# Kernel tuning notes

Measured on AMD Instinct MI355X. Metric: run time of the kernel, lower is better.

## Reference

```python
import jax, jax.numpy as jnp
import numpy as np

HID = 1024
DEPTH = 2

def _rhn_layer(x, Win, bin_, Wh, bh, Wt, bt):
    # x: [B, T, in]; returns outputs [B, T, H]
    B = x.shape[0]
    h0 = jnp.zeros((B, HID), dtype=x.dtype)
    xt = jnp.swapaxes(x, 0, 1)  # [T, B, in]

    def step(h_prev, x_t):
        h = x_t @ Win + bin_
        for i in range(DEPTH):
            t_gate = jax.nn.sigmoid(h @ Wt[i] + bt[i])
            h_layer = jnp.tanh(h @ Wh[i] + bh[i])
            h = t_gate * h_layer + (1.0 - t_gate) * h
        h_new = h + h_prev
        return h_new, h_new

    _, outs = jax.lax.scan(step, h0, xt)  # [T, B, H]
    return jnp.swapaxes(outs, 0, 1)


def setup_inputs() -> dict:
    key = jax.random.key(0)
    ks = jax.random.split(key, 16)
    B, T, IN, H, OUT = 64, 256, 128, HID, 128
    s = lambda fan_in: 1.0 / np.sqrt(fan_in)
    d = {}
    d["x"] = jax.random.normal(ks[0], (B, T, IN), dtype=jnp.float32)
    # layer 0 (input_size=IN)
    d["l0_Win"] = jax.random.uniform(ks[1], (IN, H), minval=-s(IN), maxval=s(IN))
    d["l0_bin"] = jax.random.uniform(ks[2], (H,), minval=-s(IN), maxval=s(IN))
    d["l0_Wh"] = jax.random.uniform(ks[3], (DEPTH, H, H), minval=-s(H), maxval=s(H))
    d["l0_bh"] = jax.random.uniform(ks[4], (DEPTH, H), minval=-s(H), maxval=s(H))
    d["l0_Wt"] = jax.random.uniform(ks[5], (DEPTH, H, H), minval=-s(H), maxval=s(H))
    d["l0_bt"] = jax.random.uniform(ks[6], (DEPTH, H), minval=-s(H), maxval=s(H))
    # layer 1 (input_size=H)
    d["l1_Win"] = jax.random.uniform(ks[7], (H, H), minval=-s(H), maxval=s(H))
    d["l1_bin"] = jax.random.uniform(ks[8], (H,), minval=-s(H), maxval=s(H))
    d["l1_Wh"] = jax.random.uniform(ks[9], (DEPTH, H, H), minval=-s(H), maxval=s(H))
    d["l1_bh"] = jax.random.uniform(ks[10], (DEPTH, H), minval=-s(H), maxval=s(H))
    d["l1_Wt"] = jax.random.uniform(ks[11], (DEPTH, H, H), minval=-s(H), maxval=s(H))
    d["l1_bt"] = jax.random.uniform(ks[12], (DEPTH, H), minval=-s(H), maxval=s(H))
    # final fc
    d["fc_W"] = jax.random.uniform(ks[13], (H, OUT), minval=-s(H), maxval=s(H))
    d["fc_b"] = jax.random.uniform(ks[14], (OUT,), minval=-s(H), maxval=s(H))
    return d


def reference(x, l0_Win, l0_bin, l0_Wh, l0_bh, l0_Wt, l0_bt,
              l1_Win, l1_bin, l1_Wh, l1_bh, l1_Wt, l1_bt, fc_W, fc_b):
    out = _rhn_layer(x, l0_Win, l0_bin, l0_Wh, l0_bh, l0_Wt, l0_bt)
    out = _rhn_layer(out, l1_Win, l1_bin, l1_Wh, l1_bh, l1_Wt, l1_bt)
    # forecast_horizon = 1 -> last time step only
    out = out[:, -1:, :] @ fc_W + fc_b  # [B, 1, OUT]
    return out
```

## Files before the change

kernel.cpp:

```cpp
#include <hip/hip_runtime.h>

typedef unsigned short u16;
typedef unsigned int u32;
typedef __bf16 bf16x8 __attribute__((ext_vector_type(8)));
typedef float floatx4 __attribute__((ext_vector_type(4)));

#define HID 1024
#define BATCH 64
#define SEQ 256
#define INDIM 128
#define OUTDIM 128
#define MROWS (BATCH*SEQ)

__device__ __forceinline__ float b2f(u16 u) {
    union { u32 u; float f; } v; v.u = ((u32)u) << 16; return v.f;
}
__device__ __forceinline__ u16 f2b(float f) {
    union { float f; u32 u; } v; v.f = f;
    u32 x = v.u;
    x += 0x7fffu + ((x >> 16) & 1u);
    return (u16)(x >> 16);
}
__device__ __forceinline__ float sigm(float x) { return 1.f / (1.f + __expf(-x)); }
__device__ __forceinline__ float tanh_f(float x) { return 2.f / (1.f + __expf(-2.f * x)) - 1.f; }

__device__ __forceinline__ void gld16(const u16* g, u16* l) {
    __builtin_amdgcn_global_load_lds(
        (const __attribute__((address_space(1))) void*)g,
        (__attribute__((address_space(3))) void*)l, 16, 0, 0);
}

__device__ __forceinline__ void bar_sync() {
    asm volatile("" ::: "memory");
    __builtin_amdgcn_s_barrier();
    asm volatile("" ::: "memory");
}
template <int N>
__device__ __forceinline__ void vm_bar() {
    asm volatile("s_waitcnt vmcnt(%0)" :: "n"(N) : "memory");
    __builtin_amdgcn_s_barrier();
    asm volatile("" ::: "memory");
}

__global__ void detect_dtype(const u16* __restrict__ w, int* __restrict__ flag) {
    __shared__ int s;
    if (threadIdx.x == 0) s = 0;
    __syncthreads();
    int bad = 0;
    for (int i = threadIdx.x; i < 4096; i += 256) {
        int e = (w[i] >> 7) & 0xff;
        if (e >= 127) bad = 1;
    }
    if (bad) atomicOr(&s, 1);
    __syncthreads();
    if (threadIdx.x == 0) *flag = s;
}

__device__ __forceinline__ int is_fp32(const u16* probe) {
    const int lane = threadIdx.x & 63;
    const int e = (probe[lane * 7] >> 7) & 0xff;
    return __ballot(e >= 127) != 0ULL;
}

struct CvtList { const void* s[7]; u16* d[7]; int n[7]; };

__global__ void convert7(CvtList C, const int* __restrict__ flag) {
    const int fp32 = *flag;
    const int z = blockIdx.y;
    const int n = C.n[z];
    const int stride = gridDim.x * 256;
    for (int i = blockIdx.x * 256 + threadIdx.x; i < n; i += stride) {
        u16 o;
        if (fp32) o = f2b(((const float*)C.s[z])[i]);
        else      o = ((const u16*)C.s[z])[i];
        C.d[z][i] = o;
    }
}

struct TListO {
    const void* s[10];
    u16*        d[10];
    int         R[10];
    int         Cc[10];
    long        off[10];
};

__global__ void transpose10(TListO L, const int* __restrict__ flag) {
    const int fp32 = *flag;
    const int z = blockIdx.z;
    const void* src = L.s[z];
    u16*        dst = L.d[z];
    const int R  = L.R[z];
    const int Cc = L.Cc[z];
    const long zo = L.off[z];
    const int tr = blockIdx.y * 32, tc = blockIdx.x * 32;
    if (tr >= R || tc >= Cc) return;
    __align__(16) __shared__ u16 t[32][33];
    const int tx = threadIdx.x, ty = threadIdx.y;
#pragma unroll
    for (int i = 0; i < 4; ++i) {
        const int r = ty + i * 8;
        const long e = zo + (long)(tr + r) * Cc + tc + tx;
        u16 v;
        if (fp32) v = f2b(((const float*)src)[e]);
        else      v = ((const u16*)src)[e];
        t[r][tx] = v;
    }
    __syncthreads();
#pragma unroll
    for (int i = 0; i < 4; ++i) {
        const int r = ty + i * 8;
        dst[(size_t)(tc + r) * R + tr + tx] = t[tx][r];
    }
}

__device__ __forceinline__ void tile_swizzle(int& m0, int& n0) {
    const int lin = blockIdx.y * gridDim.x + blockIdx.x;
    const int xcd = lin & 7;
    const int loc = lin >> 3;
    m0 = (xcd * 16 + (loc & 15)) * 128;
    n0 = (loc >> 4) * 128;
}

__device__ __forceinline__ void tile_swizzle8(int& m0, int& n0) {
    const int lin = blockIdx.x;
    const int xcd = lin & 7;
    const int loc = lin >> 3;
    m0 = (xcd * 8 + (loc & 7)) * 256;
    n0 = (loc >> 3) * 128;
}

__global__ __launch_bounds__(256, 2) void gemm128(
    const u16* __restrict__ A, const u16* __restrict__ BT,
    const u16* __restrict__ bias, u16* __restrict__ C,
    int M, int N, int K)
{
    __align__(16) __shared__ u16 As[128 * 64];
    __align__(16) __shared__ u16 Bs[128 * 64];

    const int tid  = threadIdx.x;
    const int lane = tid & 63;
    const int wid  = tid >> 6;
    const int wr   = wid >> 1;
    const int wc   = wid & 1;

    int m0, n0;
    tile_swizzle(m0, n0);

    floatx4 acc[4][4] = {};

    const int srow = lane >> 3;
    const int scol = 8 * ((lane & 7) ^ (lane >> 3));
    const int cb   = wid * 4;
    const u16* Ag[4]; const u16* Bg[4];
    u16 *Al[4], *Bl[4];
#pragma unroll
    for (int j = 0; j < 4; ++j) {
        const int c = cb + j;
        const int r = c * 8 + srow;
        Ag[j] = A  + (size_t)(m0 + r) * K + scol;
        Bg[j] = BT + (size_t)(n0 + r) * K + scol;
        Al[j] = As + c * 512;
        Bl[j] = Bs + c * 512;
    }

    const int quad = lane >> 4;
    const int l16  = lane & 15;
    const int swz  = l16 & 7;

    const int nk = K >> 6;
    for (int kt = 0; kt < nk; ++kt) {
        __syncthreads();
#pragma unroll
        for (int j = 0; j < 4; ++j) {
            gld16(Ag[j], Al[j]);  gld16(Bg[j], Bl[j]);
            Ag[j] += 64; Bg[j] += 64;
        }
        __syncthreads();

#pragma unroll
        for (int kk = 0; kk < 2; ++kk) {
            const int slot = ((kk * 4 + quad) ^ swz) * 8;
            bf16x8 af[4], bfr[4];
#pragma unroll
            for (int i = 0; i < 4; ++i) {
                af[i]  = *(const bf16x8*)(As + (wr * 64 + i * 16 + l16) * 64 + slot);
                bfr[i] = *(const bf16x8*)(Bs + (wc * 64 + i * 16 + l16) * 64 + slot);
            }
#pragma unroll
            for (int i = 0; i < 4; ++i)
#pragma unroll
                for (int j = 0; j < 4; ++j)
                    acc[i][j] = __builtin_amdgcn_mfma_f32_16x16x32_bf16(af[i], bfr[j], acc[i][j], 0, 0, 0);
        }
    }

#pragma unroll
    for (int i = 0; i < 4; ++i) {
        const int rowb = m0 + wr * 64 + i * 16 + quad * 4;
#pragma unroll
        for (int j = 0; j < 4; ++j) {
            const int col = n0 + wc * 64 + j * 16 + l16;
            const float bv = b2f(bias[col]);
#pragma unroll
            for (int r = 0; r < 4; ++r)
                C[(size_t)(rowb + r) * N + col] = f2b(acc[i][j][r] + bv);
        }
    }
}

__global__ __launch_bounds__(256, 2) void gemm_hw(
    const u16* __restrict__ A,
    const u16* __restrict__ WtT,
    const u16* __restrict__ WhT,
    const u16* __restrict__ bt, const u16* __restrict__ bh,
    u16* __restrict__ Hout,
    int M, int N, int K)
{
    __align__(16) __shared__ u16 As [128 * 64];
    __align__(16) __shared__ u16 Bts[128 * 64];
    __align__(16) __shared__ u16 Bhs[128 * 64];

    const int tid  = threadIdx.x;
    const int lane = tid & 63;
    const int wid  = tid >> 6;
    const int wr   = wid >> 1;
    const int wc   = wid & 1;

    int m0, n0;
    tile_swizzle(m0, n0);

    floatx4 acct[4][4] = {};
    floatx4 acch[4][4] = {};

    const int srow = lane >> 3;
    const int scol = 8 * ((lane & 7) ^ (lane >> 3));
    const int cb   = wid * 4;
    const u16* Ag[4]; const u16* Tg[4]; const u16* Hg[4];
    u16 *Al[4], *Tl[4], *Hl[4];
#pragma unroll
    for (int j = 0; j < 4; ++j) {
        const int c = cb + j;
        const int r = c * 8 + srow;
        Ag[j] = A   + (size_t)(m0 + r) * K + scol;
        Tg[j] = WtT + (size_t)(n0 + r) * K + scol;
        Hg[j] = WhT + (size_t)(n0 + r) * K + scol;
        Al[j] = As  + c * 512;
        Tl[j] = Bts + c * 512;
        Hl[j] = Bhs + c * 512;
    }

    const int quad = lane >> 4;
    const int l16  = lane & 15;
    const int swz  = l16 & 7;

    const int nk = K >> 6;
    for (int kt = 0; kt < nk; ++kt) {
        __syncthreads();
#pragma unroll
        for (int j = 0; j < 4; ++j) {
            gld16(Ag[j], Al[j]);  gld16(Tg[j], Tl[j]);  gld16(Hg[j], Hl[j]);
            Ag[j] += 64; Tg[j] += 64; Hg[j] += 64;
        }
        __syncthreads();

#pragma unroll
        for (int kk = 0; kk < 2; ++kk) {
            const int slot = ((kk * 4 + quad) ^ swz) * 8;
            bf16x8 af[4], btf[4], bhf[4];
#pragma unroll
            for (int i = 0; i < 4; ++i) {
                af[i]  = *(const bf16x8*)(As  + (wr * 64 + i * 16 + l16) * 64 + slot);
                btf[i] = *(const bf16x8*)(Bts + (wc * 64 + i * 16 + l16) * 64 + slot);
                bhf[i] = *(const bf16x8*)(Bhs + (wc * 64 + i * 16 + l16) * 64 + slot);
            }
#pragma unroll
            for (int i = 0; i < 4; ++i)
#pragma unroll
                for (int j = 0; j < 4; ++j) {
                    acct[i][j] = __builtin_amdgcn_mfma_f32_16x16x32_bf16(af[i], btf[j], acct[i][j], 0, 0, 0);
                    acch[i][j] = __builtin_amdgcn_mfma_f32_16x16x32_bf16(af[i], bhf[j], acch[i][j], 0, 0, 0);
                }
        }
    }

#pragma unroll
    for (int i = 0; i < 4; ++i) {
        const int rowb = m0 + wr * 64 + i * 16 + quad * 4;
#pragma unroll
        for (int j = 0; j < 4; ++j) {
            const int col = n0 + wc * 64 + j * 16 + l16;
            const float btv = b2f(bt[col]);
            const float bhv = b2f(bh[col]);
#pragma unroll
            for (int r = 0; r < 4; ++r) {
                const size_t idx = (size_t)(rowb + r) * N + col;
                const float hold = b2f(A[idx]);
                const float tg = sigm(acct[i][j][r] + btv);
                const float hl = tanh_f(acch[i][j][r] + bhv);
                Hout[idx] = f2b(hold + tg * (hl - hold));
            }
        }
    }
}

__global__ __launch_bounds__(256, 2) void gemm_hw_sum(
    const u16* __restrict__ A,
    const u16* __restrict__ WtT,
    const u16* __restrict__ WhT,
    const u16* __restrict__ bt, const u16* __restrict__ bh,
    float* __restrict__ hsum,
    int M, int N, int K)
{
    __align__(16) __shared__ u16 As [128 * 64];
    __align__(16) __shared__ u16 Bts[128 * 64];
    __align__(16) __shared__ u16 Bhs[128 * 64];

    const int tid  = threadIdx.x;
    const int lane = tid & 63;
    const int wid  = tid >> 6;
    const int wr   = wid >> 1;
    const int wc   = wid & 1;

    int m0, n0;
    tile_swizzle(m0, n0);

    floatx4 acct[4][4] = {};
    floatx4 acch[4][4] = {};

    const int srow = lane >> 3;
    const int scol = 8 * ((lane & 7) ^ (lane >> 3));
    const int cb   = wid * 4;
    const u16* Ag[4]; const u16* Tg[4]; const u16* Hg[4];
    u16 *Al[4], *Tl[4], *Hl[4];
#pragma unroll
    for (int j = 0; j < 4; ++j) {
        const int c = cb + j;
        const int r = c * 8 + srow;
        Ag[j] = A   + (size_t)(m0 + r) * K + scol;
        Tg[j] = WtT + (size_t)(n0 + r) * K + scol;
        Hg[j] = WhT + (size_t)(n0 + r) * K + scol;
        Al[j] = As  + c * 512;
        Tl[j] = Bts + c * 512;
        Hl[j] = Bhs + c * 512;
    }

    const int quad = lane >> 4;
    const int l16  = lane & 15;
    const int swz  = l16 & 7;

    const int nk = K >> 6;
    for (int kt = 0; kt < nk; ++kt) {
        __syncthreads();
#pragma unroll
        for (int j = 0; j < 4; ++j) {
            gld16(Ag[j], Al[j]);  gld16(Tg[j], Tl[j]);  gld16(Hg[j], Hl[j]);
            Ag[j] += 64; Tg[j] += 64; Hg[j] += 64;
        }
        __syncthreads();

#pragma unroll
        for (int kk = 0; kk < 2; ++kk) {
            const int slot = ((kk * 4 + quad) ^ swz) * 8;
            bf16x8 af[4], btf[4], bhf[4];
#pragma unroll
            for (int i = 0; i < 4; ++i) {
                af[i]  = *(const bf16x8*)(As  + (wr * 64 + i * 16 + l16) * 64 + slot);
                btf[i] = *(const bf16x8*)(Bts + (wc * 64 + i * 16 + l16) * 64 + slot);
                bhf[i] = *(const bf16x8*)(Bhs + (wc * 64 + i * 16 + l16) * 64 + slot);
            }
#pragma unroll
            for (int i = 0; i < 4; ++i)
#pragma unroll
                for (int j = 0; j < 4; ++j) {
                    acct[i][j] = __builtin_amdgcn_mfma_f32_16x16x32_bf16(af[i], btf[j], acct[i][j], 0, 0, 0);
                    acch[i][j] = __builtin_amdgcn_mfma_f32_16x16x32_bf16(af[i], bhf[j], acch[i][j], 0, 0, 0);
                }
        }
    }

    const int b = m0 >> 8;
#pragma unroll
    for (int j = 0; j < 4; ++j) {
        const int col = n0 + wc * 64 + j * 16 + l16;
        const float btv = b2f(bt[col]);
        const float bhv = b2f(bh[col]);
        float colsum = 0.f;
#pragma unroll
        for (int i = 0; i < 4; ++i) {
            const int rowb = m0 + wr * 64 + i * 16 + quad * 4;
#pragma unroll
            for (int r = 0; r < 4; ++r) {
                const size_t idx = (size_t)(rowb + r) * N + col;
                const float hold = b2f(A[idx]);
                const float tg = sigm(acct[i][j][r] + btv);
                const float hl = tanh_f(acch[i][j][r] + bhv);
                colsum += hold + tg * (hl - hold);
            }
        }
        colsum += __shfl_xor(colsum, 16, 64);
        colsum += __shfl_xor(colsum, 32, 64);
        if (quad == 0)
            atomicAdd(&hsum[(size_t)b * HID + col], colsum);
    }
}

__device__ __forceinline__ void hw8_mainloop(
    u16* lds,
    const u16* __restrict__ A, const u16* __restrict__ WtT, const u16* __restrict__ WhT,
    int m0, int n0, int K,
    floatx4 (&acct)[4][4], floatx4 (&acch)[4][4])
{
    const int tid  = threadIdx.x;
    const int lane = tid & 63;
    const int wid  = tid >> 6;
    const int wr   = wid >> 1;
    const int wc   = wid & 1;

    const int srow = lane >> 3;
    const int scol = 8 * ((lane & 7) ^ srow);

    const u16* Ag = A   + (size_t)(m0 + wid * 32 + srow) * K + scol;
    const u16* Tg = WtT + (size_t)(n0 + wid * 16 + srow) * K + scol;
    const u16* Hg = WhT + (size_t)(n0 + wid * 16 + srow) * K + scol;
    const size_t K8 = (size_t)K * 8;

    u16* dA = lds + wid * 2048;
    u16* dT = lds + 16384 + wid * 1024;
    u16* dH = lds + 24576 + wid * 1024;

    const int quad = lane >> 4;
    const int l16  = lane & 15;
    const int swz  = l16 & 7;
    const int s0 = (quad ^ swz) * 8;
    const int s1 = ((4 + quad) ^ swz) * 8;
    const int ra = wr * 64 + l16;
    const int rb = wc * 64 + l16;

    gld16(Tg,           dT);
    gld16(Tg +     K8,  dT + 512);
    gld16(Ag,           dA);
    gld16(Ag +     K8,  dA + 512);
    gld16(Ag + 2 * K8,  dA + 1024);
    gld16(Ag + 3 * K8,  dA + 1536);
    gld16(Hg,           dH);
    gld16(Hg +     K8,  dH + 512);
    Ag += 64; Tg += 64; Hg += 64;
    vm_bar<2>();

    const int nk = K >> 6;
    for (int kt = 0; kt < nk; ++kt) {
        const int  cur = kt & 1;
        const int  nb  = (cur ^ 1) * 32768;
        const bool pf  = (kt + 1 < nk);
        const u16* Sa = lds + cur * 32768;
        const u16* St = Sa + 16384;
        const u16* Sh = Sa + 24576;

        bf16x8 af0[4], af1[4], bq[4];

#pragma unroll
        for (int i = 0; i < 4; ++i) {
            af0[i] = *(const bf16x8*)(Sa + (ra + i * 16) * 64 + s0);
            bq[i]  = *(const bf16x8*)(St + (rb + i * 16) * 64 + s0);
        }
        if (pf) {
            gld16(Tg,      dT + nb);  gld16(Tg + K8, dT + nb + 512);
            gld16(Ag,      dA + nb);  gld16(Ag + K8, dA + nb + 512);
        }
        bar_sync();
        __builtin_amdgcn_s_setprio(1);
#pragma unroll
        for (int i = 0; i < 4; ++i)
#pragma unroll
            for (int j = 0; j < 4; ++j)
                acct[i][j] = __builtin_amdgcn_mfma_f32_16x16x32_bf16(af0[i], bq[j], acct[i][j], 0, 0, 0);
        __builtin_amdgcn_s_setprio(0);

#pragma unroll
        for (int i = 0; i < 4; ++i) {
            af1[i] = *(const bf16x8*)(Sa + (ra + i * 16) * 64 + s1);
            bq[i]  = *(const bf16x8*)(St + (rb + i * 16) * 64 + s1);
        }
        if (pf) {
            gld16(Ag + 2 * K8, dA + nb + 1024);
            gld16(Ag + 3 * K8, dA + nb + 1536);
            vm_bar<6>();
        } else {
            vm_bar<0>();
        }
        __builtin_amdgcn_s_setprio(1);
#pragma unroll
        for (int i = 0; i < 4; ++i)
#pragma unroll
            for (int j = 0; j < 4; ++j)
                acct[i][j] = __builtin_amdgcn_mfma_f32_16x16x32_bf16(af1[i], bq[j], acct[i][j], 0, 0, 0);
        __builtin_amdgcn_s_setprio(0);

#pragma unroll
        for (int i = 0; i < 4; ++i)
            bq[i] = *(const bf16x8*)(Sh + (rb + i * 16) * 64 + s0);
        bar_sync();
        __builtin_amdgcn_s_setprio(1);
#pragma unroll
        for (int i = 0; i < 4; ++i)
#pragma unroll
            for (int j = 0; j < 4; ++j)
                acch[i][j] = __builtin_amdgcn_mfma_f32_16x16x32_bf16(af0[i], bq[j], acch[i][j], 0, 0, 0);
        __builtin_amdgcn_s_setprio(0);

#pragma unroll
        for (int i = 0; i < 4; ++i)
            bq[i] = *(const bf16x8*)(Sh + (rb + i * 16) * 64 + s1);
        if (pf) {
            gld16(Hg,      dH + nb);
            gld16(Hg + K8, dH + nb + 512);
            vm_bar<2>();
        } else {
            bar_sync();
        }
        __builtin_amdgcn_s_setprio(1);
#pragma unroll
        for (int i = 0; i < 4; ++i)
#pragma unroll
            for (int j = 0; j < 4; ++j)
                acch[i][j] = __builtin_amdgcn_mfma_f32_16x16x32_bf16(af1[i], bq[j], acch[i][j], 0, 0, 0);
        __builtin_amdgcn_s_setprio(0);

        Ag += 64; Tg += 64; Hg += 64;
    }
}

__global__ __launch_bounds__(512, 2) void gemm_hw8_cum(
    const u16* __restrict__ A,
    const u16* __restrict__ WtT,
    const u16* __restrict__ WhT,
    const u16* __restrict__ bt, const u16* __restrict__ bh,
    u16* __restrict__ Y,
    int M, int N, int K)
{
    __align__(16) __shared__ u16 lds[65536];

    int m0, n0;
    tile_swizzle8(m0, n0);

    floatx4 acct[4][4] = {};
    floatx4 acch[4][4] = {};
    hw8_mainloop(lds, A, WtT, WhT, m0, n0, K, acct, acch);

    const int tid  = threadIdx.x;
    const int lane = tid & 63;
    const int wid  = tid >> 6;
    const int wr   = wid >> 1;
    const int wc   = wid & 1;
    const int quad = lane >> 4;
    const int l16  = lane & 15;

    __syncthreads();

#pragma unroll
    for (int i = 0; i < 4; ++i) {
        const int rowl = wr * 64 + i * 16 + quad * 4;
#pragma unroll
        for (int j = 0; j < 4; ++j) {
            const int coll = wc * 64 + j * 16 + l16;
            const float btv = b2f(bt[n0 + coll]);
            const float bhv = b2f(bh[n0 + coll]);
#pragma unroll
            for (int r = 0; r < 4; ++r) {
                const size_t idx = (size_t)(m0 + rowl + r) * N + n0 + coll;
                const float hold = b2f(A[idx]);
                const float tg = sigm(acct[i][j][r] + btv);
                const float hl = tanh_f(acch[i][j][r] + bhv);
                lds[(rowl + r) * 128 + coll] = f2b(hold + tg * (hl - hold));
            }
        }
    }
    __syncthreads();

    if (tid < 128) {
        float acc = 0.f;
#pragma unroll 8
        for (int t = 0; t < SEQ; ++t) {
            const int o = t * 128 + tid;
            acc += b2f(lds[o]);
            lds[o] = f2b(acc);
        }
    }
    __syncthreads();

#pragma unroll
    for (int it = 0; it < 16; ++it) {
        const int o   = it * 2048 + tid * 4;
        const int row = o >> 7;
        const int col = o & 127;
        *(uint2*)&Y[(size_t)(m0 + row) * N + n0 + col] = *(const uint2*)&lds[o];
    }
}

__global__ void zero_hf(float* __restrict__ p) {
    p[blockIdx.x * 256 + threadIdx.x] = 0.f;
}

__global__ void fc_final(const float* __restrict__ hf, const void* __restrict__ W,
                         const void* __restrict__ bias, void* __restrict__ out) {
    __shared__ float sh[HID];
    const int fp32 = is_fp32((const u16*)W);
    const int b = blockIdx.x, o = threadIdx.x;
    for (int k = o; k < HID; k += 128) sh[k] = hf[(size_t)b * HID + k];
    __syncthreads();
    float acc;
    if (fp32) {
        acc = ((const float*)bias)[o];
        for (int k = 0; k < HID; ++k)
            acc += sh[k] * ((const float*)W)[(size_t)k * OUTDIM + o];
        ((float*)out)[b * OUTDIM + o] = acc;
    } else {
        acc = b2f(((const u16*)bias)[o]);
        for (int k = 0; k < HID; ++k)
            acc += sh[k] * b2f(((const u16*)W)[(size_t)k * OUTDIM + o]);
        ((u16*)out)[b * OUTDIM + o] = f2b(acc);
    }
}

extern "C" void kernel_launch(void* const* d_in, const int* in_sizes, int n_in,
                              void* d_out, int out_size, void* d_ws, size_t ws_size,
                              hipStream_t stream) {
    const void* x      = d_in[0];
    const void* l0_Win = d_in[1];
    const void* l0_bin = d_in[2];
    const void* l0_Wh  = d_in[3];
    const void* l0_bh  = d_in[4];
    const void* l0_Wt  = d_in[5];
    const void* l0_bt  = d_in[6];
    const void* l1_Win = d_in[7];
    const void* l1_bin = d_in[8];
    const void* l1_Wh  = d_in[9];
    const void* l1_bh  = d_in[10];
    const void* l1_Wt  = d_in[11];
    const void* l1_bt  = d_in[12];
    const void* fc_W   = d_in[13];
    const void* fc_b   = d_in[14];

    char* ws = (char*)d_ws;
    u16* Pa = (u16*)(ws);
    u16* Pb = (u16*)(ws + 33554432);
    u16* xc = Pb;
    u16* tW = (u16*)(ws + 67108864);
    u16* tWin0 = tW;
    u16* tWt00 = tWin0 + 131072;
    u16* tWt01 = tWt00 + 1048576;
    u16* tWh00 = tWt01 + 1048576;
    u16* tWh01 = tWh00 + 1048576;
    u16* tWin1 = tWh01 + 1048576;
    u16* tWt10 = tWin1 + 1048576;
    u16* tWt11 = tWt10 + 1048576;
    u16* tWh10 = tWt11 + 1048576;
    u16* tWh11 = tWh10 + 1048576;
    u16* smallb = tWh11 + 1048576;
    u16* binc0 = smallb;
    u16* bhc0  = binc0 + 1024;
    u16* btc0  = bhc0 + 2048;
    u16* binc1 = btc0 + 2048;
    u16* bhc1  = binc1 + 1024;
    u16* btc1  = bhc1 + 2048;
    int* flag  = (int*)(btc1 + 2048);
    float* hfinal = (float*)Pb;

    detect_dtype<<<1, 256, 0, stream>>>((const u16*)l0_Wh, flag);

    const long DD = (long)HID * HID;
    TListO L;
    L.s[0] = l0_Win; L.d[0] = tWin0; L.R[0] = INDIM; L.Cc[0] = HID; L.off[0] = 0;
    L.s[1] = l0_Wt;  L.d[1] = tWt00; L.R[1] = HID;   L.Cc[1] = HID; L.off[1] = 0;
    L.s[2] = l0_Wt;  L.d[2] = tWt01; L.R[2] = HID;   L.Cc[2] = HID; L.off[2] = DD;
    L.s[3] = l0_Wh;  L.d[3] = tWh00; L.R[3] = HID;   L.Cc[3] = HID; L.off[3] = 0;
    L.s[4] = l0_Wh;  L.d[4] = tWh01; L.R[4] = HID;   L.Cc[4] = HID; L.off[4] = DD;
    L.s[5] = l1_Win; L.d[5] = tWin1; L.R[5] = HID;   L.Cc[5] = HID; L.off[5] = 0;
    L.s[6] = l1_Wt;  L.d[6] = tWt10; L.R[6] = HID;   L.Cc[6] = HID; L.off[6] = 0;
    L.s[7] = l1_Wt;  L.d[7] = tWt11; L.R[7] = HID;   L.Cc[7] = HID; L.off[7] = DD;
    L.s[8] = l1_Wh;  L.d[8] = tWh10; L.R[8] = HID;   L.Cc[8] = HID; L.off[8] = 0;
    L.s[9] = l1_Wh;  L.d[9] = tWh11; L.R[9] = HID;   L.Cc[9] = HID; L.off[9] = DD;
    transpose10<<<dim3(32, 32, 10), dim3(32, 8), 0, stream>>>(L, flag);

    CvtList C7;
    C7.s[0] = x;      C7.d[0] = xc;    C7.n[0] = MROWS * INDIM;
    C7.s[1] = l0_bin; C7.d[1] = binc0; C7.n[1] = HID;
    C7.s[2] = l0_bh;  C7.d[2] = bhc0;  C7.n[2] = 2 * HID;
    C7.s[3] = l0_bt;  C7.d[3] = btc0;  C7.n[3] = 2 * HID;
    C7.s[4] = l1_bin; C7.d[4] = binc1; C7.n[4] = HID;
    C7.s[5] = l1_bh;  C7.d[5] = bhc1;  C7.n[5] = 2 * HID;
    C7.s[6] = l1_bt;  C7.d[6] = btc1;  C7.n[6] = 2 * HID;
    convert7<<<dim3(512, 7), 256, 0, stream>>>(C7, flag);

    gemm128<<<dim3(8, 128), 256, 0, stream>>>(xc, tWin0, binc0, Pa, MROWS, HID, INDIM);
    gemm_hw<<<dim3(8, 128), 256, 0, stream>>>(Pa, tWt00, tWh00, btc0, bhc0, Pb, MROWS, HID, HID);
    gemm_hw8_cum<<<512, 512, 0, stream>>>(Pb, tWt01, tWh01, btc0 + HID, bhc0 + HID, Pa, MROWS, HID, HID);

    gemm128<<<dim3(8, 128), 256, 0, stream>>>(Pa, tWin1, binc1, Pb, MROWS, HID, HID);
    gemm_hw<<<dim3(8, 128), 256, 0, stream>>>(Pb, tWt10, tWh10, btc1, bhc1, Pa, MROWS, HID, HID);
    zero_hf<<<256, 256, 0, stream>>>(hfinal);
    gemm_hw_sum<<<dim3(8, 128), 256, 0, stream>>>(Pa, tWt11, tWh11, btc1 + HID, bhc1 + HID,
                                                  hfinal, MROWS, HID, HID);

    fc_final<<<64, 128, 0, stream>>>(hfinal, fc_W, fc_b, d_out);
}
```

Measured before the change: 526.8 us.

## Parallelize cumulative scan, drop dtype/zero kernels, replace atomics with partial sums

Removes the separate dtype-detect kernel by having each kernel probe the dtype inline with a wave ballot. Drops the zero-fill kernel by writing per-tile column partial sums to distinct slots that fc_final adds up, instead of using atomics. The time-axis prefix sum in gemm_hw8_cum now uses all 512 threads in four 64-step segments with a two-pass offset scheme instead of 128 threads walking 256 steps. The LDS row stride is padded to 140 to reduce bank conflicts. The cost is extra LDS use and a small repeated probe load in every block.

New measurement: 520.0 us. Within noise of the previous version (-1.3%).

```diff
diff --git a/kernel.cpp b/kernel.cpp
--- a/kernel.cpp
+++ b/kernel.cpp
@@ -11,6 +11,7 @@
 #define INDIM 128
 #define OUTDIM 128
 #define MROWS (BATCH*SEQ)
+#define CUMP 140
 
 __device__ __forceinline__ float b2f(u16 u) {
     union { u32 u; float f; } v; v.u = ((u32)u) << 16; return v.f;
@@ -42,30 +43,16 @@
     asm volatile("" ::: "memory");
 }
 
-__global__ void detect_dtype(const u16* __restrict__ w, int* __restrict__ flag) {
-    __shared__ int s;
-    if (threadIdx.x == 0) s = 0;
-    __syncthreads();
-    int bad = 0;
-    for (int i = threadIdx.x; i < 4096; i += 256) {
-        int e = (w[i] >> 7) & 0xff;
-        if (e >= 127) bad = 1;
-    }
-    if (bad) atomicOr(&s, 1);
-    __syncthreads();
-    if (threadIdx.x == 0) *flag = s;
-}
-
-__device__ __forceinline__ int is_fp32(const u16* probe) {
-    const int lane = threadIdx.x & 63;
+__device__ __forceinline__ int is_fp32(const u16* probe, int tid) {
+    const int lane = tid & 63;
     const int e = (probe[lane * 7] >> 7) & 0xff;
     return __ballot(e >= 127) != 0ULL;
 }
 
 struct CvtList { const void* s[7]; u16* d[7]; int n[7]; };
 
-__global__ void convert7(CvtList C, const int* __restrict__ flag) {
-    const int fp32 = *flag;
+__global__ void convert7(CvtList C, const u16* __restrict__ probe) {
+    const int fp32 = is_fp32(probe, threadIdx.x);
     const int z = blockIdx.y;
     const int n = C.n[z];
     const int stride = gridDim.x * 256;
@@ -85,8 +72,9 @@
     long        off[10];
 };
 
-__global__ void transpose10(TListO L, const int* __restrict__ flag) {
-    const int fp32 = *flag;
+__global__ void transpose10(TListO L, const u16* __restrict__ probe) {
+    const int tx = threadIdx.x, ty = threadIdx.y;
+    const int fp32 = is_fp32(probe, ty * 32 + tx);
     const int z = blockIdx.z;
     const void* src = L.s[z];
     u16*        dst = L.d[z];
@@ -96,7 +84,6 @@
     const int tr = blockIdx.y * 32, tc = blockIdx.x * 32;
     if (tr >= R || tc >= Cc) return;
     __align__(16) __shared__ u16 t[32][33];
-    const int tx = threadIdx.x, ty = threadIdx.y;
 #pragma unroll
     for (int i = 0; i < 4; ++i) {
         const int r = ty + i * 8;
@@ -309,7 +296,7 @@
     const u16* __restrict__ WtT,
     const u16* __restrict__ WhT,
     const u16* __restrict__ bt, const u16* __restrict__ bh,
-    float* __restrict__ hsum,
+    float* __restrict__ hpart,
     int M, int N, int K)
 {
     __align__(16) __shared__ u16 As [128 * 64];
@@ -379,7 +366,8 @@
         }
     }
 
-    const int b = m0 >> 8;
+    const int b    = m0 >> 8;
+    const int slot = ((m0 >> 7) & 1) * 2 + wr;
 #pragma unroll
     for (int j = 0; j < 4; ++j) {
         const int col = n0 + wc * 64 + j * 16 + l16;
@@ -401,7 +389,7 @@
         colsum += __shfl_xor(colsum, 16, 64);
         colsum += __shfl_xor(colsum, 32, 64);
         if (quad == 0)
-            atomicAdd(&hsum[(size_t)b * HID + col], colsum);
+            hpart[((size_t)(slot * BATCH + b)) * HID + col] = colsum;
     }
 }
 
@@ -540,6 +528,7 @@
     int M, int N, int K)
 {
     __align__(16) __shared__ u16 lds[65536];
+    __shared__ float tot[512];
 
     int m0, n0;
     tile_swizzle8(m0, n0);
@@ -572,17 +561,32 @@
                 const float hold = b2f(A[idx]);
                 const float tg = sigm(acct[i][j][r] + btv);
                 const float hl = tanh_f(acch[i][j][r] + bhv);
-                lds[(rowl + r) * 128 + coll] = f2b(hold + tg * (hl - hold));
+                lds[(rowl + r) * CUMP + coll] = f2b(hold + tg * (hl - hold));
             }
         }
     }
     __syncthreads();
 
-    if (tid < 128) {
-        float acc = 0.f;
+    const int seg  = tid >> 7;
+    const int colc = tid & 127;
+    const int base = seg * 64 * CUMP + colc;
+    {
+        float local = 0.f;
 #pragma unroll 8
-        for (int t = 0; t < SEQ; ++t) {
-            const int o = t * 128 + tid;
+        for (int t = 0; t < 64; ++t)
+            local += b2f(lds[base + t * CUMP]);
+        tot[seg * 128 + colc] = local;
+    }
+    __syncthreads();
+    {
+        float off = 0.f;
+#pragma unroll
+        for (int s = 0; s < 3; ++s)
+            off += (s < seg) ? tot[s * 128 + colc] : 0.f;
+        float acc = off;
+#pragma unroll 8
+        for (int t = 0; t < 64; ++t) {
+            const int o = base + t * CUMP;
             acc += b2f(lds[o]);
             lds[o] = f2b(acc);
         }
@@ -594,20 +598,23 @@
         const int o   = it * 2048 + tid * 4;
         const int row = o >> 7;
         const int col = o & 127;
-        *(uint2*)&Y[(size_t)(m0 + row) * N + n0 + col] = *(const uint2*)&lds[o];
-    }
-}
-
-__global__ void zero_hf(float* __restrict__ p) {
-    p[blockIdx.x * 256 + threadIdx.x] = 0.f;
-}
-
-__global__ void fc_final(const float* __restrict__ hf, const void* __restrict__ W,
+        *(uint2*)&Y[(size_t)(m0 + row) * N + n0 + col] =
+            *(const uint2*)&lds[row * CUMP + col];
+    }
+}
+
+__global__ void fc_final(const float* __restrict__ hp, const void* __restrict__ W,
                          const void* __restrict__ bias, void* __restrict__ out) {
     __shared__ float sh[HID];
-    const int fp32 = is_fp32((const u16*)W);
+    const int fp32 = is_fp32((const u16*)W, threadIdx.x);
     const int b = blockIdx.x, o = threadIdx.x;
-    for (int k = o; k < HID; k += 128) sh[k] = hf[(size_t)b * HID + k];
+    for (int k = o; k < HID; k += 128) {
+        float v = 0.f;
+#pragma unroll
+        for (int s = 0; s < 4; ++s)
+            v += hp[((size_t)(s * BATCH + b)) * HID + k];
+        sh[k] = v;
+    }
     __syncthreads();
     float acc;
     if (fp32) {
@@ -664,10 +671,9 @@
     u16* binc1 = btc0 + 2048;
     u16* bhc1  = binc1 + 1024;
     u16* btc1  = bhc1 + 2048;
-    int* flag  = (int*)(btc1 + 2048);
-    float* hfinal = (float*)Pb;
-
-    detect_dtype<<<1, 256, 0, stream>>>((const u16*)l0_Wh, flag);
+    float* hpart = (float*)Pb;
+
+    const u16* probe = (const u16*)l0_Wh;
 
     const long DD = (long)HID * HID;
     TListO L;
@@ -681,7 +687,7 @@
     L.s[7] = l1_Wt;  L.d[7] = tWt11; L.R[7] = HID;   L.Cc[7] = HID; L.off[7] = DD;
     L.s[8] = l1_Wh;  L.d[8] = tWh10; L.R[8] = HID;   L.Cc[8] = HID; L.off[8] = 0;
     L.s[9] = l1_Wh;  L.d[9] = tWh11; L.R[9] = HID;   L.Cc[9] = HID; L.off[9] = DD;
-    transpose10<<<dim3(32, 32, 10), dim3(32, 8), 0, stream>>>(L, flag);
+    transpose10<<<dim3(32, 32, 10), dim3(32, 8), 0, stream>>>(L, probe);
 
     CvtList C7;
     C7.s[0] = x;      C7.d[0] = xc;    C7.n[0] = MROWS * INDIM;
@@ -691,7 +697,7 @@
     C7.s[4] = l1_bin; C7.d[4] = binc1; C7.n[4] = HID;
     C7.s[5] = l1_bh;  C7.d[5] = bhc1;  C7.n[5] = 2 * HID;
     C7.s[6] = l1_bt;  C7.d[6] = btc1;  C7.n[6] = 2 * HID;
-    convert7<<<dim3(512, 7), 256, 0, stream>>>(C7, flag);
+    convert7<<<dim3(512, 7), 256, 0, stream>>>(C7, probe);
 
     gemm128<<<dim3(8, 128), 256, 0, stream>>>(xc, tWin0, binc0, Pa, MROWS, HID, INDIM);
     gemm_hw<<<dim3(8, 128), 256, 0, stream>>>(Pa, tWt00, tWh00, btc0, bhc0, Pb, MROWS, HID, HID);
@@ -699,9 +705,8 @@
 
     gemm128<<<dim3(8, 128), 256, 0, stream>>>(Pa, tWin1, binc1, Pb, MROWS, HID, HID);
     gemm_hw<<<dim3(8, 128), 256, 0, stream>>>(Pb, tWt10, tWh10, btc1, bhc1, Pa, MROWS, HID, HID);
-    zero_hf<<<256, 256, 0, stream>>>(hfinal);
     gemm_hw_sum<<<dim3(8, 128), 256, 0, stream>>>(Pa, tWt11, tWh11, btc1 + HID, bhc1 + HID,
-                                                  hfinal, MROWS, HID, HID);
-
-    fc_final<<<64, 128, 0, stream>>>(hfinal, fc_W, fc_b, d_out);
-}
+                                                  hpart, MROWS, HID, HID);
+
+    fc_final<<<64, 128, 0, stream>>>(hpart, fc_W, fc_b, d_out);
+}
```
